# Performance work log

Hardware: AMD Instinct MI355X
Metric: run time of the kernel (lower is better)

The kernel has to match this reference:

```python
import jax, jax.numpy as jnp
import numpy as np
from jax import lax

B, T, D, LD, K = 128, 1024, 256, 512, 128
RD = LD + K  # 640 residual-LSTM width
PAD = 15     # (31 - 1) // 2 'same' padding for the LSA location conv


def _gru(x, h, wih, whh, bih, bhh):
    # torch.nn.GRUCell semantics, gate order [r, z, n]
    gi = x @ wih.T + bih
    gh = h @ whh.T + bhh
    ir, iz, inn = jnp.split(gi, 3, axis=-1)
    hr, hz, hn = jnp.split(gh, 3, axis=-1)
    r = jax.nn.sigmoid(ir + hr)
    z = jax.nn.sigmoid(iz + hz)
    n = jnp.tanh(inn + r * hn)
    return (1.0 - z) * n + z * h


def _lstm(x, h, c, wih, whh, bih, bhh):
    # torch.nn.LSTMCell semantics, gate order [i, f, g, o]
    g = x @ wih.T + bih + h @ whh.T + bhh
    i, f, gg, o = jnp.split(g, 4, axis=-1)
    c2 = jax.nn.sigmoid(f) * c + jax.nn.sigmoid(i) * jnp.tanh(gg)
    h2 = jax.nn.sigmoid(o) * jnp.tanh(c2)
    return h2, c2


def _forward(encoder_seq, encoder_seq_proj, prenet_in, attn_hidden, rnn1_h, rnn1_c,
             rnn2_h, rnn2_c, res_h, res_c, context_vec, cumulative, attn_prev,
             fc1_w, fc1_b, fc2_w, fc2_b, gru_wih, gru_whh, gru_bih, gru_bhh,
             conv_w, L_w, L_b, W_w, W_b, v_w, ri_w, ri_b,
             r1_wih, r1_whh, r1_bih, r1_bhh, r2_wih, r2_whh, r2_bih, r2_bhh,
             res_wih, res_whh, res_bih, res_bhh, stop_w, stop_b):
    # PreNet (dropout p = 0 in Decoder.__init__, so pure tanh-MLP)
    p = jnp.tanh(prenet_in @ fc1_w.T + fc1_b)
    prenet_out = jnp.tanh(p @ fc2_w.T + fc2_b)                     # [B, D//2]
    # Attention GRU
    attn_in = jnp.concatenate([context_vec, prenet_out], axis=-1)  # [B, D + D//2]
    attn_h = _gru(attn_in, attn_hidden, gru_wih, gru_whh, gru_bih, gru_bhh)  # [B, D]
    # LSA location-sensitive attention (cumulative/attn_prev are zeros at t=0)
    pq = (attn_h @ W_w.T + W_b)[:, None, :]                        # [B, 1, D]
    loc = jnp.stack([cumulative, attn_prev], axis=1)               # [B, 2, T]
    conv_out = lax.conv_general_dilated(loc, conv_w, (1,), [(PAD, PAD)],
                                        dimension_numbers=('NCH', 'OIH', 'NCH'))  # [B, 32, T]
    ploc = jnp.swapaxes(conv_out, 1, 2) @ L_w.T + L_b              # [B, T, D]
    u = jnp.squeeze(jnp.tanh(pq + encoder_seq_proj + ploc) @ v_w.T, -1)  # [B, T]
    sig = jax.nn.sigmoid(u)
    scores = sig / jnp.sum(sig, axis=1, keepdims=True)             # [B, T]
    cum_new = cumulative + scores
    context = jnp.einsum('bt,btd->bd', scores, encoder_seq)        # [B, D]
    # rnn_input projection + two residual LSTM cells (eval: no zoneout)
    x = jnp.concatenate([context, attn_h], axis=1) @ ri_w.T + ri_b  # [B, LD]
    h1, c1 = _lstm(x, rnn1_h, rnn1_c, r1_wih, r1_whh, r1_bih, r1_bhh)
    x = x + h1
    h2, c2 = _lstm(x, rnn2_h, rnn2_c, r2_wih, r2_whh, r2_bih, r2_bhh)
    x = x + h2
    # 4-layer residual LSTM stack on [prenet_in, x]
    res_x = jnp.concatenate([prenet_in, x], axis=1)                # [B, RD]
    hs, cs = [], []
    for i in range(4):
        hi, ci = _lstm(res_x, res_h[i], res_c[i], res_wih[i], res_whh[i], res_bih[i], res_bhh[i])
        res_x = res_x + hi
        hs.append(hi)
        cs.append(ci)
    cond = res_x                                                   # cond_features [B, RD]
    stop = jax.nn.sigmoid(cond @ stop_w.T + stop_b)                # [B, 1]
    return (cond, stop, scores, attn_h, h1, c1, h2, c2,
            jnp.stack(hs), jnp.stack(cs), context, cum_new)


def setup_inputs() -> dict:
    keys = iter(jax.random.split(jax.random.key(0), 64))
    nxt = lambda: next(keys)
    rn = lambda s: jax.random.normal(nxt(), s, jnp.float32)
    wp = lambda s: rn(s) * 0.02
    return {
        'encoder_seq': rn((B, T, D)),
        'encoder_seq_proj': rn((B, T, D)),
        'prenet_in': rn((B, K)),
        'attn_hidden': rn((B, D)),
        'rnn1_h': rn((B, LD)), 'rnn1_c': rn((B, LD)),
        'rnn2_h': rn((B, LD)), 'rnn2_c': rn((B, LD)),
        'res_h': rn((4, B, RD)), 'res_c': rn((4, B, RD)),
        'context_vec': rn((B, D)),
        'cumulative': jnp.zeros((B, T), jnp.float32),
        'attn_prev': jnp.zeros((B, T), jnp.float32),
        'fc1_w': wp((256, K)), 'fc1_b': jnp.zeros((256,), jnp.float32),
        'fc2_w': wp((D // 2, 256)), 'fc2_b': jnp.zeros((D // 2,), jnp.float32),
        'gru_wih': wp((3 * D, D + D // 2)), 'gru_whh': wp((3 * D, D)),
        'gru_bih': jnp.zeros((3 * D,), jnp.float32), 'gru_bhh': jnp.zeros((3 * D,), jnp.float32),
        'conv_w': wp((32, 2, 31)),
        'L_w': wp((D, 32)), 'L_b': jnp.zeros((D,), jnp.float32),
        'W_w': wp((D, D)), 'W_b': jnp.zeros((D,), jnp.float32),
        'v_w': wp((1, D)),
        'ri_w': wp((LD, 2 * D)), 'ri_b': jnp.zeros((LD,), jnp.float32),
        'r1_wih': wp((4 * LD, LD)), 'r1_whh': wp((4 * LD, LD)),
        'r1_bih': jnp.zeros((4 * LD,), jnp.float32), 'r1_bhh': jnp.zeros((4 * LD,), jnp.float32),
        'r2_wih': wp((4 * LD, LD)), 'r2_whh': wp((4 * LD, LD)),
        'r2_bih': jnp.zeros((4 * LD,), jnp.float32), 'r2_bhh': jnp.zeros((4 * LD,), jnp.float32),
        'res_wih': wp((4, 4 * RD, RD)), 'res_whh': wp((4, 4 * RD, RD)),
        'res_bih': jnp.zeros((4, 4 * RD), jnp.float32), 'res_bhh': jnp.zeros((4, 4 * RD), jnp.float32),
        'stop_w': wp((1, RD)), 'stop_b': jnp.zeros((1,), jnp.float32),
    }


def reference(encoder_seq, encoder_seq_proj, prenet_in, attn_hidden, rnn1_h, rnn1_c,
              rnn2_h, rnn2_c, res_h, res_c, context_vec, cumulative, attn_prev,
              fc1_w, fc1_b, fc2_w, fc2_b, gru_wih, gru_whh, gru_bih, gru_bhh,
              conv_w, L_w, L_b, W_w, W_b, v_w, ri_w, ri_b,
              r1_wih, r1_whh, r1_bih, r1_bhh, r2_wih, r2_whh, r2_bih, r2_bhh,
              res_wih, res_whh, res_bih, res_bhh, stop_w, stop_b):
    return _forward(encoder_seq, encoder_seq_proj, prenet_in, attn_hidden, rnn1_h, rnn1_c,
                    rnn2_h, rnn2_c, res_h, res_c, context_vec, cumulative, attn_prev,
                    fc1_w, fc1_b, fc2_w, fc2_b, gru_wih, gru_whh, gru_bih, gru_bhh,
                    conv_w, L_w, L_b, W_w, W_b, v_w, ri_w, ri_b,
                    r1_wih, r1_whh, r1_bih, r1_bhh, r2_wih, r2_whh, r2_bih, r2_bhh,
                    res_wih, res_whh, res_bih, res_bhh, stop_w, stop_b)
```

## Files before the change

kernel.cpp:

```cpp
#include <hip/hip_runtime.h>

#define DEV __device__ __forceinline__

typedef __attribute__((ext_vector_type(8))) short short8;
typedef __attribute__((ext_vector_type(4))) float f32x4;

DEV float fast_rcp(float x) { return __builtin_amdgcn_rcpf(x); }
DEV float sigm(float x) { return fast_rcp(1.0f + __expf(-x)); }
DEV float tanhf_fast(float x) { return 1.0f - 2.0f * fast_rcp(1.0f + __expf(2.0f * x)); }

DEV short f2bf(float f) {
    unsigned u = __float_as_uint(f);
    unsigned r = (u + 0x7FFFu + ((u >> 16) & 1u)) >> 16;
    return (short)r;
}

__global__ __launch_bounds__(256) void gemm2s_kernel(
    const float* __restrict__ A1, int K1, const float* __restrict__ W1, int ldw1,
    const float* __restrict__ A2, int K2, const float* __restrict__ W2, int ldw2,
    float* __restrict__ Cp, int N, int KS, int KC)
{
    __shared__ float As[2][16][128];
    __shared__ float Ws[2][16][33];
    const int tid = threadIdx.x;
    const int chunk = blockIdx.x % KS;
    const int n0 = (blockIdx.x / KS) * 32;
    const int kbeg = chunk * KC;
    const int nt = KC / 16;
    const int tx = tid & 15, ty = tid >> 4;
    const int lm = tid & 127, lk = (tid >> 7) * 8;

    float acc[16];
#pragma unroll
    for (int i = 0; i < 16; ++i) acc[i] = 0.f;

    float4 ra0, ra1, rw;
    auto load_regs = [&](int k0) {
        const float* A; const float* W; int lda, ldw, kc;
        if (k0 < K1) { A = A1; W = W1; lda = K1; ldw = ldw1; kc = k0; }
        else         { A = A2; W = W2; lda = K2; ldw = ldw2; kc = k0 - K1; }
        ra0 = *(const float4*)(A + (size_t)lm * lda + kc + lk);
        ra1 = *(const float4*)(A + (size_t)lm * lda + kc + lk + 4);
        if (tid < 128) {
            int nl = tid >> 2, kq = (tid & 3) * 4;
            rw = *(const float4*)(W + (size_t)(n0 + nl) * ldw + kc + kq);
        }
    };
    auto store_lds = [&](int buf) {
        As[buf][lk + 0][lm] = ra0.x; As[buf][lk + 1][lm] = ra0.y;
        As[buf][lk + 2][lm] = ra0.z; As[buf][lk + 3][lm] = ra0.w;
        As[buf][lk + 4][lm] = ra1.x; As[buf][lk + 5][lm] = ra1.y;
        As[buf][lk + 6][lm] = ra1.z; As[buf][lk + 7][lm] = ra1.w;
        if (tid < 128) {
            int nl = tid >> 2, kq = (tid & 3) * 4;
            Ws[buf][kq + 0][nl] = rw.x; Ws[buf][kq + 1][nl] = rw.y;
            Ws[buf][kq + 2][nl] = rw.z; Ws[buf][kq + 3][nl] = rw.w;
        }
    };

    load_regs(kbeg);
    store_lds(0);
    __syncthreads();

    for (int it = 0; it < nt; ++it) {
        const int cur = it & 1;
        if (it + 1 < nt) load_regs(kbeg + (it + 1) * 16);
#pragma unroll
        for (int kk = 0; kk < 16; ++kk) {
            float w0 = Ws[cur][kk][tx * 2 + 0];
            float w1 = Ws[cur][kk][tx * 2 + 1];
            float4 x0 = *(const float4*)&As[cur][kk][ty * 8];
            float4 x1 = *(const float4*)&As[cur][kk][ty * 8 + 4];
            acc[0] += x0.x * w0; acc[1] += x0.y * w0;
            acc[2] += x0.z * w0; acc[3] += x0.w * w0;
            acc[4] += x1.x * w0; acc[5] += x1.y * w0;
            acc[6] += x1.z * w0; acc[7] += x1.w * w0;
            acc[8]  += x0.x * w1; acc[9]  += x0.y * w1;
            acc[10] += x0.z * w1; acc[11] += x0.w * w1;
            acc[12] += x1.x * w1; acc[13] += x1.y * w1;
            acc[14] += x1.z * w1; acc[15] += x1.w * w1;
        }
        if (it + 1 < nt) store_lds(cur ^ 1);
        __syncthreads();
    }

    float* Co = Cp + (size_t)chunk * 128 * N;
#pragma unroll
    for (int j = 0; j < 2; ++j) {
        int n = n0 + tx * 2 + j;
#pragma unroll
        for (int i = 0; i < 8; ++i)
            Co[(size_t)(ty * 8 + i) * N + n] = acc[j * 8 + i];
    }
}

__global__ void reduce_act_kernel(const float* __restrict__ p, int KS, int MN,
                                  const float* __restrict__ b,
                                  float* __restrict__ out, int N, int act)
{
    int idx = blockIdx.x * 256 + threadIdx.x;
    if (idx >= MN) return;
    int n = idx % N;
    float v = b ? b[n] : 0.f;
    for (int s = 0; s < KS; ++s) v += p[(size_t)s * MN + idx];
    if (act) v = tanhf_fast(v);
    out[idx] = v;
}

__global__ void gru_gate_kernel(const float* __restrict__ gi_p, int KSi,
                                const float* __restrict__ gh_p, int KSh,
                                const float* __restrict__ bih, const float* __restrict__ bhh,
                                const float* __restrict__ h, float* __restrict__ out)
{
    const size_t MN = 128 * 768;
    int m = blockIdx.x, d = threadIdx.x;
    size_t base = (size_t)m * 768 + d;
    float ir = bih[d], iz = bih[256 + d], in = bih[512 + d];
    for (int s = 0; s < KSi; ++s) {
        const float* p = gi_p + s * MN + base;
        ir += p[0]; iz += p[256]; in += p[512];
    }
    float hr = bhh[d], hz = bhh[256 + d], hn = bhh[512 + d];
    for (int s = 0; s < KSh; ++s) {
        const float* p = gh_p + s * MN + base;
        hr += p[0]; hz += p[256]; hn += p[512];
    }
    float r = sigm(ir + hr);
    float z = sigm(iz + hz);
    float n = tanhf_fast(in + r * hn);
    out[m * 256 + d] = (1.f - z) * n + z * h[m * 256 + d];
}

__global__ void lstm_gate_kernel(const float* __restrict__ gp, int KS,
                                 const float* __restrict__ bih, const float* __restrict__ bhh,
                                 const float* __restrict__ c_in,
                                 float* __restrict__ h_out, float* __restrict__ c_out,
                                 float* __restrict__ xacc, int H)
{
    int d = blockIdx.x * 256 + threadIdx.x;
    int m = blockIdx.y;
    if (d >= H) return;
    const size_t MN = (size_t)128 * 4 * H;
    size_t base = (size_t)m * 4 * H + d;
    float iv = bih[d] + bhh[d];
    float fv = bih[H + d] + bhh[H + d];
    float gv = bih[2 * H + d] + bhh[2 * H + d];
    float ov = bih[3 * H + d] + bhh[3 * H + d];
    for (int s = 0; s < KS; ++s) {
        const float* p = gp + s * MN + base;
        iv += p[0]; fv += p[H]; gv += p[2 * H]; ov += p[3 * H];
    }
    float c2 = sigm(fv) * c_in[m * H + d] + sigm(iv) * tanhf_fast(gv);
    float h2 = sigm(ov) * tanhf_fast(c2);
    h_out[m * H + d] = h2;
    c_out[m * H + d] = c2;
    if (xacc) xacc[m * H + d] += h2;
}

__global__ void lw_bf16_kernel(const float* __restrict__ Lw, short* __restrict__ LwBf)
{
    int i = blockIdx.x * 256 + threadIdx.x;
    LwBf[i] = f2bf(Lw[i]);
}

__global__ __launch_bounds__(256) void attn_u_kernel(
    const float* __restrict__ esp, const float* __restrict__ pq,
    const short* __restrict__ LwBf, const float* __restrict__ Lb,
    const float* __restrict__ vw, const float* __restrict__ cw,
    const float* __restrict__ cum, const float* __restrict__ prev,
    float* __restrict__ sig_out)
{
    const int b = blockIdx.x >> 4;
    const int t0 = (blockIdx.x & 15) << 6;
    const int tid = threadIdx.x;

    __shared__ float cum_s[94], prev_s[94];
    __shared__ float cw_s[2][32][33];
    __shared__ short conv_bf[64 * 32];
    __shared__ short lw_bf[256 * 32];
    __shared__ float pq_s[256], vw_s[256];

    if (tid < 94) {
        int ti = t0 - 15 + tid;
        cum_s[tid] = (ti >= 0 && ti < 1024) ? cum[b * 1024 + ti] : 0.f;
    } else if (tid >= 128 && tid < 222) {
        int i = tid - 128;
        int ti = t0 - 15 + i;
        prev_s[i] = (ti >= 0 && ti < 1024) ? prev[b * 1024 + ti] : 0.f;
    }
    for (int i = tid; i < 2048; i += 256) {
        int which = i >> 10, c = (i >> 5) & 31, k = i & 31;
        cw_s[which][c][k] = (k < 31) ? cw[(c * 2 + which) * 31 + k] : 0.f;
    }
    {
        const int4* src = (const int4*)LwBf;
        int4* dst = (int4*)lw_bf;
#pragma unroll
        for (int k = 0; k < 4; ++k) dst[tid + k * 256] = src[tid + k * 256];
    }
    pq_s[tid] = pq[b * 256 + tid] + Lb[tid];
    vw_s[tid] = vw[tid];
    __syncthreads();

    {
        int c = tid & 31, t8 = (tid >> 5) << 3;
        float a[8] = {0.f, 0.f, 0.f, 0.f, 0.f, 0.f, 0.f, 0.f};
        for (int k = 0; k < 31; ++k) {
            float w0 = cw_s[0][c][k], w1 = cw_s[1][c][k];
#pragma unroll
            for (int j = 0; j < 8; ++j)
                a[j] += w0 * cum_s[t8 + j + k] + w1 * prev_s[t8 + j + k];
        }
#pragma unroll
        for (int j = 0; j < 8; ++j) conv_bf[(t8 + j) * 32 + c] = f2bf(a[j]);
    }
    __syncthreads();

    const int lane = tid & 63, w = tid >> 6;
    const int q = lane >> 4, c16 = lane & 15;
    const int myt = t0 + w * 16 + c16;

    short8 bfrag = *(const short8*)&conv_bf[(w * 16 + c16) * 32 + q * 8];
    const float* er = esp + ((size_t)(b * 1024 + myt) << 8);

    float s = 0.f;
#pragma unroll
    for (int dt = 0; dt < 16; ++dt) {
        short8 afrag = *(const short8*)&lw_bf[(dt * 16 + c16) * 32 + q * 8];
        f32x4 acc = {0.f, 0.f, 0.f, 0.f};
        acc = __builtin_amdgcn_mfma_f32_16x16x32_bf16(afrag, bfrag, acc, 0, 0, 0);
        const int d0 = dt * 16 + q * 4;
        float4 e   = *(const float4*)(er + d0);
        float4 pqv = *(const float4*)&pq_s[d0];
        float4 vwv = *(const float4*)&vw_s[d0];
        s += tanhf_fast(pqv.x + e.x + acc[0]) * vwv.x;
        s += tanhf_fast(pqv.y + e.y + acc[1]) * vwv.y;
        s += tanhf_fast(pqv.z + e.z + acc[2]) * vwv.z;
        s += tanhf_fast(pqv.w + e.w + acc[3]) * vwv.w;
    }
    s += __shfl_xor(s, 16);
    s += __shfl_xor(s, 32);
    if (lane < 16)
        sig_out[b * 1024 + t0 + w * 16 + lane] = sigm(s);
}

__global__ void attn_norm_kernel(const float* __restrict__ sig, const float* __restrict__ cum,
                                 float* __restrict__ scores, float* __restrict__ cum_new,
                                 float* __restrict__ ctx)
{
    __shared__ float red[4];
    int b = blockIdx.x, tid = threadIdx.x;
    float4 sv = *(const float4*)&sig[b * 1024 + tid * 4];
    float s = sv.x + sv.y + sv.z + sv.w;
#pragma unroll
    for (int off = 1; off < 64; off <<= 1) s += __shfl_xor(s, off);
    if ((tid & 63) == 0) red[tid >> 6] = s;
    __syncthreads();
    float inv = fast_rcp(red[0] + red[1] + red[2] + red[3]);
    float4 cv = *(const float4*)&cum[b * 1024 + tid * 4];
    float4 sc = {sv.x * inv, sv.y * inv, sv.z * inv, sv.w * inv};
    *(float4*)&scores[b * 1024 + tid * 4] = sc;
    float4 cn = {cv.x + sc.x, cv.y + sc.y, cv.z + sc.z, cv.w + sc.w};
    *(float4*)&cum_new[b * 1024 + tid * 4] = cn;
    ctx[b * 256 + tid] = 0.f;
}

__global__ void attn_ctx_kernel(const float* __restrict__ scores, const float* __restrict__ es,
                                float* __restrict__ ctx)
{
    __shared__ float sc_s[128];
    int b = blockIdx.x >> 3;
    int tbase = (blockIdx.x & 7) * 128;
    int tid = threadIdx.x;
    if (tid < 128) sc_s[tid] = scores[b * 1024 + tbase + tid];
    __syncthreads();
    float a = 0.f;
    const float* ep = es + ((size_t)(b * 1024 + tbase)) * 256 + tid;
#pragma unroll 4
    for (int tt = 0; tt < 128; ++tt)
        a += sc_s[tt] * ep[(size_t)tt * 256];
    atomicAdd(&ctx[b * 256 + tid], a);
}

__global__ void build_rescat_kernel(const float* __restrict__ pre, const float* __restrict__ x,
                                    float* __restrict__ res)
{
    int idx = blockIdx.x * 256 + threadIdx.x;
    int m = idx / 640, d = idx - m * 640;
    res[idx] = (d < 128) ? pre[m * 128 + d] : x[m * 512 + d - 128];
}

__global__ void copy_kernel(const float* __restrict__ src, float* __restrict__ dst, int n)
{
    int idx = blockIdx.x * 256 + threadIdx.x;
    if (idx < n) dst[idx] = src[idx];
}

__global__ void stop_kernel(const float* __restrict__ res, const float* __restrict__ sw,
                            const float* __restrict__ sb, float* __restrict__ stop)
{
    int m = blockIdx.x, lane = threadIdx.x;
    float s = 0.f;
    for (int k = lane; k < 640; k += 64) s += res[m * 640 + k] * sw[k];
#pragma unroll
    for (int off = 1; off < 64; off <<= 1) s += __shfl_xor(s, off);
    if (lane == 0) stop[m] = sigm(s + sb[0]);
}

extern "C" void kernel_launch(void* const* d_in, const int* in_sizes, int n_in,
                              void* d_out, int out_size, void* d_ws, size_t ws_size,
                              hipStream_t stream)
{
    const float* encoder_seq      = (const float*)d_in[0];
    const float* encoder_seq_proj = (const float*)d_in[1];
    const float* prenet_in        = (const float*)d_in[2];
    const float* attn_hidden      = (const float*)d_in[3];
    const float* rnn1_h  = (const float*)d_in[4];
    const float* rnn1_c  = (const float*)d_in[5];
    const float* rnn2_h  = (const float*)d_in[6];
    const float* rnn2_c  = (const float*)d_in[7];
    const float* res_h   = (const float*)d_in[8];
    const float* res_c   = (const float*)d_in[9];
    const float* context_vec = (const float*)d_in[10];
    const float* cumulative  = (const float*)d_in[11];
    const float* attn_prev   = (const float*)d_in[12];
    const float* fc1_w = (const float*)d_in[13];
    const float* fc1_b = (const float*)d_in[14];
    const float* fc2_w = (const float*)d_in[15];
    const float* fc2_b = (const float*)d_in[16];
    const float* gru_wih = (const float*)d_in[17];
    const float* gru_whh = (const float*)d_in[18];
    const float* gru_bih = (const float*)d_in[19];
    const float* gru_bhh = (const float*)d_in[20];
    const float* conv_w = (const float*)d_in[21];
    const float* L_w = (const float*)d_in[22];
    const float* L_b = (const float*)d_in[23];
    const float* W_w = (const float*)d_in[24];
    const float* W_b = (const float*)d_in[25];
    const float* v_w = (const float*)d_in[26];
    const float* ri_w = (const float*)d_in[27];
    const float* ri_b = (const float*)d_in[28];
    const float* r1_wih = (const float*)d_in[29];
    const float* r1_whh = (const float*)d_in[30];
    const float* r1_bih = (const float*)d_in[31];
    const float* r1_bhh = (const float*)d_in[32];
    const float* r2_wih = (const float*)d_in[33];
    const float* r2_whh = (const float*)d_in[34];
    const float* r2_bih = (const float*)d_in[35];
    const float* r2_bhh = (const float*)d_in[36];
    const float* res_wih = (const float*)d_in[37];
    const float* res_whh = (const float*)d_in[38];
    const float* res_bih = (const float*)d_in[39];
    const float* res_bhh = (const float*)d_in[40];
    const float* stop_w = (const float*)d_in[41];
    const float* stop_b = (const float*)d_in[42];

    float* ws  = (float*)d_ws;
    float* out = (float*)d_out;

    const size_t OFF_P    = 0;
    const size_t OFF_POUT = 32768;
    const size_t OFF_PQ   = 49152;
    const size_t OFF_SIG  = 81920;
    const size_t OFF_X    = 212992;
    const size_t OFF_RES  = 278528;
    const size_t OFF_LWT  = 360448;
    const size_t OFF_PART = 368640;
    const size_t OFF_PARTB = OFF_PART + (size_t)8 * 128 * 768;

    const size_t O_COND   = 0;
    const size_t O_STOP   = 81920;
    const size_t O_SCORES = 82048;
    const size_t O_ATTNH  = 213120;
    const size_t O_H1     = 245888;
    const size_t O_C1     = 311424;
    const size_t O_H2     = 376960;
    const size_t O_C2     = 442496;
    const size_t O_HS     = 508032;
    const size_t O_CS     = 835712;
    const size_t O_CTX    = 1163392;
    const size_t O_CUM    = 1196160;

    short* lwbf = (short*)(ws + OFF_LWT);
    lw_bf16_kernel<<<32, 256, 0, stream>>>(L_w, lwbf);

    gemm2s_kernel<<<8 * 4, 256, 0, stream>>>(prenet_in, 128, fc1_w, 128,
                                             nullptr, 0, nullptr, 0,
                                             ws + OFF_PART, 256, 4, 32);
    reduce_act_kernel<<<128, 256, 0, stream>>>(ws + OFF_PART, 4, 128 * 256, fc1_b,
                                               ws + OFF_P, 256, 1);
    gemm2s_kernel<<<4 * 8, 256, 0, stream>>>(ws + OFF_P, 256, fc2_w, 256,
                                             nullptr, 0, nullptr, 0,
                                             ws + OFF_PART, 128, 8, 32);
    reduce_act_kernel<<<64, 256, 0, stream>>>(ws + OFF_PART, 8, 128 * 128, fc2_b,
                                              ws + OFF_POUT, 128, 1);

    gemm2s_kernel<<<24 * 8, 256, 0, stream>>>(context_vec, 256, gru_wih, 384,
                                              ws + OFF_POUT, 128, gru_wih + 256, 384,
                                              ws + OFF_PART, 768, 8, 48);
    gemm2s_kernel<<<24 * 8, 256, 0, stream>>>(attn_hidden, 256, gru_whh, 256,
                                              nullptr, 0, nullptr, 0,
                                              ws + OFF_PARTB, 768, 8, 32);
    gru_gate_kernel<<<128, 256, 0, stream>>>(ws + OFF_PART, 8, ws + OFF_PARTB, 8,
                                             gru_bih, gru_bhh, attn_hidden, out + O_ATTNH);

    gemm2s_kernel<<<8 * 8, 256, 0, stream>>>(out + O_ATTNH, 256, W_w, 256,
                                             nullptr, 0, nullptr, 0,
                                             ws + OFF_PART, 256, 8, 32);
    reduce_act_kernel<<<128, 256, 0, stream>>>(ws + OFF_PART, 8, 128 * 256, W_b,
                                               ws + OFF_PQ, 256, 0);

    attn_u_kernel<<<2048, 256, 0, stream>>>(encoder_seq_proj, ws + OFF_PQ, lwbf,
                                            L_b, v_w, conv_w, cumulative, attn_prev,
                                            ws + OFF_SIG);
    attn_norm_kernel<<<128, 256, 0, stream>>>(ws + OFF_SIG, cumulative,
                                              out + O_SCORES, out + O_CUM, out + O_CTX);
    attn_ctx_kernel<<<1024, 256, 0, stream>>>(out + O_SCORES, encoder_seq, out + O_CTX);

    gemm2s_kernel<<<16 * 8, 256, 0, stream>>>(out + O_CTX, 256, ri_w, 512,
                                              out + O_ATTNH, 256, ri_w + 256, 512,
                                              ws + OFF_PART, 512, 8, 64);
    reduce_act_kernel<<<256, 256, 0, stream>>>(ws + OFF_PART, 8, 128 * 512, ri_b,
                                               ws + OFF_X, 512, 0);

    gemm2s_kernel<<<64 * 8, 256, 0, stream>>>(ws + OFF_X, 512, r1_wih, 512,
                                              rnn1_h, 512, r1_whh, 512,
                                              ws + OFF_PART, 2048, 8, 128);
    lstm_gate_kernel<<<dim3(2, 128), 256, 0, stream>>>(ws + OFF_PART, 8, r1_bih, r1_bhh,
                                                       rnn1_c, out + O_H1, out + O_C1,
                                                       ws + OFF_X, 512);
    gemm2s_kernel<<<64 * 8, 256, 0, stream>>>(ws + OFF_X, 512, r2_wih, 512,
                                              rnn2_h, 512, r2_whh, 512,
                                              ws + OFF_PART, 2048, 8, 128);
    lstm_gate_kernel<<<dim3(2, 128), 256, 0, stream>>>(ws + OFF_PART, 8, r2_bih, r2_bhh,
                                                       rnn2_c, out + O_H2, out + O_C2,
                                                       ws + OFF_X, 512);

    build_rescat_kernel<<<320, 256, 0, stream>>>(prenet_in, ws + OFF_X, ws + OFF_RES);

    for (int i = 0; i < 4; ++i) {
        const float* wih = res_wih + (size_t)i * 2560 * 640;
        const float* whh = res_whh + (size_t)i * 2560 * 640;
        gemm2s_kernel<<<80 * 8, 256, 0, stream>>>(ws + OFF_RES, 640, wih, 640,
                                                  res_h + (size_t)i * 81920, 640, whh, 640,
                                                  ws + OFF_PART, 2560, 8, 160);
        lstm_gate_kernel<<<dim3(3, 128), 256, 0, stream>>>(ws + OFF_PART, 8,
                                                           res_bih + (size_t)i * 2560,
                                                           res_bhh + (size_t)i * 2560,
                                                           res_c + (size_t)i * 81920,
                                                           out + O_HS + (size_t)i * 81920,
                                                           out + O_CS + (size_t)i * 81920,
                                                           ws + OFF_RES, 640);
    }

    copy_kernel<<<320, 256, 0, stream>>>(ws + OFF_RES, out + O_COND, 128 * 640);
    stop_kernel<<<128, 64, 0, stream>>>(ws + OFF_RES, stop_w, stop_b, out + O_STOP);
}
```

Before: 662.4 us.

## Replace FP32 SIMT GEMM with split-bf16 MFMA GEMM using pre-converted weights

Replaces the LDS-tiled FP32 FMA GEMM with an MFMA kernel that emulates fp32 accuracy by splitting each operand into bf16 hi and lo parts and issuing three bf16 MFMAs per tile. A new kernel converts every weight matrix to hi/lo bf16 arrays each call, and the GEMM loads fragments straight from global memory with register double-buffering instead of staging through LDS. The intent is to move the matmul work onto the matrix cores. In exchange, the weight conversion pass reads about 73 MB of fp32 and writes the same volume back as bf16 every call, which is extra memory traffic. The GRU input GEMM split is also changed to 12 K-chunks.

Result: faster. 634.2 us (-4.3%).

```diff
diff --git a/kernel.cpp b/kernel.cpp
--- a/kernel.cpp
+++ b/kernel.cpp
@@ -14,84 +14,131 @@
     unsigned r = (u + 0x7FFFu + ((u >> 16) & 1u)) >> 16;
     return (short)r;
 }
-
-__global__ __launch_bounds__(256) void gemm2s_kernel(
-    const float* __restrict__ A1, int K1, const float* __restrict__ W1, int ldw1,
-    const float* __restrict__ A2, int K2, const float* __restrict__ W2, int ldw2,
+DEV float bf2f(short h) {
+    return __uint_as_float(((unsigned)(unsigned short)h) << 16);
+}
+DEV void split1(float f, short& h, short& l) {
+    h = f2bf(f);
+    l = f2bf(f - bf2f(h));
+}
+
+__global__ __launch_bounds__(256) void convert_w_kernel(
+    const float* __restrict__ p0, const float* __restrict__ p1,
+    const float* __restrict__ p2, const float* __restrict__ p3,
+    const float* __restrict__ p4, const float* __restrict__ p5,
+    const float* __restrict__ p6, const float* __restrict__ p7,
+    const float* __restrict__ p8, const float* __restrict__ p9,
+    const float* __restrict__ p10, const float* __restrict__ p11,
+    short* __restrict__ hi, short* __restrict__ lo)
+{
+    const int c1 = 8192, c2 = 16384, c3 = 90112, c4 = 139264, c5 = 155648,
+              c6 = 221184, c7 = 483328, c8 = 745472, c9 = 1007616,
+              c10 = 1269760, c11 = 2908160, total = 4546560;
+    for (int v = blockIdx.x * 256 + threadIdx.x; v < total; v += gridDim.x * 256) {
+        const float* s = p0; int base = 0;
+        if (v >= c1)  { s = p1;  base = c1; }
+        if (v >= c2)  { s = p2;  base = c2; }
+        if (v >= c3)  { s = p3;  base = c3; }
+        if (v >= c4)  { s = p4;  base = c4; }
+        if (v >= c5)  { s = p5;  base = c5; }
+        if (v >= c6)  { s = p6;  base = c6; }
+        if (v >= c7)  { s = p7;  base = c7; }
+        if (v >= c8)  { s = p8;  base = c8; }
+        if (v >= c9)  { s = p9;  base = c9; }
+        if (v >= c10) { s = p10; base = c10; }
+        if (v >= c11) { s = p11; base = c11; }
+        float4 f = ((const float4*)s)[v - base];
+        short4 h, l;
+        split1(f.x, h.x, l.x);
+        split1(f.y, h.y, l.y);
+        split1(f.z, h.z, l.z);
+        split1(f.w, h.w, l.w);
+        ((short4*)hi)[v] = h;
+        ((short4*)lo)[v] = l;
+    }
+}
+
+__global__ __launch_bounds__(256) void gemm_mfma_kernel(
+    const float* __restrict__ A1, int K1,
+    const short* __restrict__ W1hi, const short* __restrict__ W1lo, int ldw1,
+    const float* __restrict__ A2, int K2,
+    const short* __restrict__ W2hi, const short* __restrict__ W2lo, int ldw2,
     float* __restrict__ Cp, int N, int KS, int KC)
 {
-    __shared__ float As[2][16][128];
-    __shared__ float Ws[2][16][33];
     const int tid = threadIdx.x;
     const int chunk = blockIdx.x % KS;
     const int n0 = (blockIdx.x / KS) * 32;
     const int kbeg = chunk * KC;
-    const int nt = KC / 16;
-    const int tx = tid & 15, ty = tid >> 4;
-    const int lm = tid & 127, lk = (tid >> 7) * 8;
-
-    float acc[16];
-#pragma unroll
-    for (int i = 0; i < 16; ++i) acc[i] = 0.f;
-
-    float4 ra0, ra1, rw;
-    auto load_regs = [&](int k0) {
-        const float* A; const float* W; int lda, ldw, kc;
-        if (k0 < K1) { A = A1; W = W1; lda = K1; ldw = ldw1; kc = k0; }
-        else         { A = A2; W = W2; lda = K2; ldw = ldw2; kc = k0 - K1; }
-        ra0 = *(const float4*)(A + (size_t)lm * lda + kc + lk);
-        ra1 = *(const float4*)(A + (size_t)lm * lda + kc + lk + 4);
-        if (tid < 128) {
-            int nl = tid >> 2, kq = (tid & 3) * 4;
-            rw = *(const float4*)(W + (size_t)(n0 + nl) * ldw + kc + kq);
+    const int w = tid >> 6, lane = tid & 63;
+    const int q = lane >> 4, r = lane & 15;
+    const int m_base = w * 32;
+
+    f32x4 acc[2][2];
+#pragma unroll
+    for (int mt = 0; mt < 2; ++mt)
+#pragma unroll
+        for (int nt = 0; nt < 2; ++nt)
+            acc[mt][nt] = (f32x4){0.f, 0.f, 0.f, 0.f};
+
+    auto load_frag = [&](int kg, float4 (&a)[2][2], short8 (&bh)[2], short8 (&bl)[2]) {
+        const float* A; const short *Wh, *Wl; int lda, ldw, kc;
+        if (kg < K1) { A = A1; Wh = W1hi; Wl = W1lo; lda = K1; ldw = ldw1; kc = kg; }
+        else         { A = A2; Wh = W2hi; Wl = W2lo; lda = K2; ldw = ldw2; kc = kg - K1; }
+#pragma unroll
+        for (int mt = 0; mt < 2; ++mt) {
+            const float* ap = A + (size_t)(m_base + mt * 16 + r) * lda + kc + q * 8;
+            a[mt][0] = *(const float4*)ap;
+            a[mt][1] = *(const float4*)(ap + 4);
+        }
+#pragma unroll
+        for (int nt = 0; nt < 2; ++nt) {
+            size_t off = (size_t)(n0 + nt * 16 + r) * ldw + kc + q * 8;
+            bh[nt] = *(const short8*)(Wh + off);
+            bl[nt] = *(const short8*)(Wl + off);
         }
     };
-    auto store_lds = [&](int buf) {
-        As[buf][lk + 0][lm] = ra0.x; As[buf][lk + 1][lm] = ra0.y;
-        As[buf][lk + 2][lm] = ra0.z; As[buf][lk + 3][lm] = ra0.w;
-        As[buf][lk + 4][lm] = ra1.x; As[buf][lk + 5][lm] = ra1.y;
-        As[buf][lk + 6][lm] = ra1.z; As[buf][lk + 7][lm] = ra1.w;
-        if (tid < 128) {
-            int nl = tid >> 2, kq = (tid & 3) * 4;
-            Ws[buf][kq + 0][nl] = rw.x; Ws[buf][kq + 1][nl] = rw.y;
-            Ws[buf][kq + 2][nl] = rw.z; Ws[buf][kq + 3][nl] = rw.w;
+
+    auto compute = [&](const float4 (&a)[2][2], const short8 (&bh)[2], const short8 (&bl)[2]) {
+#pragma unroll
+        for (int mt = 0; mt < 2; ++mt) {
+            float fv[8] = {a[mt][0].x, a[mt][0].y, a[mt][0].z, a[mt][0].w,
+                           a[mt][1].x, a[mt][1].y, a[mt][1].z, a[mt][1].w};
+            short8 ah, al;
+#pragma unroll
+            for (int j = 0; j < 8; ++j) {
+                short h, l;
+                split1(fv[j], h, l);
+                ah[j] = h; al[j] = l;
+            }
+#pragma unroll
+            for (int nt = 0; nt < 2; ++nt) {
+                acc[mt][nt] = __builtin_amdgcn_mfma_f32_16x16x32_bf16(ah, bh[nt], acc[mt][nt], 0, 0, 0);
+                acc[mt][nt] = __builtin_amdgcn_mfma_f32_16x16x32_bf16(al, bh[nt], acc[mt][nt], 0, 0, 0);
+                acc[mt][nt] = __builtin_amdgcn_mfma_f32_16x16x32_bf16(ah, bl[nt], acc[mt][nt], 0, 0, 0);
+            }
         }
     };
 
-    load_regs(kbeg);
-    store_lds(0);
-    __syncthreads();
-
-    for (int it = 0; it < nt; ++it) {
-        const int cur = it & 1;
-        if (it + 1 < nt) load_regs(kbeg + (it + 1) * 16);
-#pragma unroll
-        for (int kk = 0; kk < 16; ++kk) {
-            float w0 = Ws[cur][kk][tx * 2 + 0];
-            float w1 = Ws[cur][kk][tx * 2 + 1];
-            float4 x0 = *(const float4*)&As[cur][kk][ty * 8];
-            float4 x1 = *(const float4*)&As[cur][kk][ty * 8 + 4];
-            acc[0] += x0.x * w0; acc[1] += x0.y * w0;
-            acc[2] += x0.z * w0; acc[3] += x0.w * w0;
-            acc[4] += x1.x * w0; acc[5] += x1.y * w0;
-            acc[6] += x1.z * w0; acc[7] += x1.w * w0;
-            acc[8]  += x0.x * w1; acc[9]  += x0.y * w1;
-            acc[10] += x0.z * w1; acc[11] += x0.w * w1;
-            acc[12] += x1.x * w1; acc[13] += x1.y * w1;
-            acc[14] += x1.z * w1; acc[15] += x1.w * w1;
-        }
-        if (it + 1 < nt) store_lds(cur ^ 1);
-        __syncthreads();
-    }
+    float4 a0[2][2], a1[2][2];
+    short8 bh0[2], bl0[2], bh1[2], bl1[2];
+    const int nsteps = KC >> 5;
+
+    load_frag(kbeg, a0, bh0, bl0);
+    for (int s = 0; s + 1 < nsteps; ++s) {
+        if (s & 1) { load_frag(kbeg + (s + 1) * 32, a0, bh0, bl0); compute(a1, bh1, bl1); }
+        else       { load_frag(kbeg + (s + 1) * 32, a1, bh1, bl1); compute(a0, bh0, bl0); }
+    }
+    if ((nsteps - 1) & 1) compute(a1, bh1, bl1);
+    else                  compute(a0, bh0, bl0);
 
     float* Co = Cp + (size_t)chunk * 128 * N;
 #pragma unroll
-    for (int j = 0; j < 2; ++j) {
-        int n = n0 + tx * 2 + j;
-#pragma unroll
-        for (int i = 0; i < 8; ++i)
-            Co[(size_t)(ty * 8 + i) * N + n] = acc[j * 8 + i];
-    }
+    for (int mt = 0; mt < 2; ++mt)
+#pragma unroll
+        for (int nt = 0; nt < 2; ++nt)
+#pragma unroll
+            for (int i = 0; i < 4; ++i)
+                Co[(size_t)(m_base + mt * 16 + q * 4 + i) * N + n0 + nt * 16 + r] = acc[mt][nt][i];
 }
 
 __global__ void reduce_act_kernel(const float* __restrict__ p, int KS, int MN,
@@ -366,7 +413,16 @@
     const size_t OFF_RES  = 278528;
     const size_t OFF_LWT  = 360448;
     const size_t OFF_PART = 368640;
-    const size_t OFF_PARTB = OFF_PART + (size_t)8 * 128 * 768;
+    const size_t OFF_PARTB = OFF_PART + (size_t)12 * 128 * 768;
+    const size_t OFF_WBF  = 4000000;
+
+    const size_t WOFF_FC1 = 0,        WOFF_FC2 = 32768,   WOFF_GI = 65536,
+                 WOFF_GH  = 360448,   WOFF_WW  = 557056,  WOFF_RI = 622592,
+                 WOFF_R1I = 884736,   WOFF_R1H = 1933312, WOFF_R2I = 2981888,
+                 WOFF_R2H = 4030464,  WOFF_RESI = 5079040, WOFF_RESH = 11632640,
+                 W_TOTAL  = 18186240;
+    short* WHI = (short*)(ws + OFF_WBF);
+    short* WLO = WHI + W_TOTAL;
 
     const size_t O_COND   = 0;
     const size_t O_STOP   = 81920;
@@ -381,32 +437,41 @@
     const size_t O_CTX    = 1163392;
     const size_t O_CUM    = 1196160;
 
+    convert_w_kernel<<<2048, 256, 0, stream>>>(
+        fc1_w, fc2_w, gru_wih, gru_whh, W_w, ri_w,
+        r1_wih, r1_whh, r2_wih, r2_whh, res_wih, res_whh, WHI, WLO);
+
     short* lwbf = (short*)(ws + OFF_LWT);
     lw_bf16_kernel<<<32, 256, 0, stream>>>(L_w, lwbf);
 
-    gemm2s_kernel<<<8 * 4, 256, 0, stream>>>(prenet_in, 128, fc1_w, 128,
-                                             nullptr, 0, nullptr, 0,
-                                             ws + OFF_PART, 256, 4, 32);
+    gemm_mfma_kernel<<<8 * 4, 256, 0, stream>>>(
+        prenet_in, 128, WHI + WOFF_FC1, WLO + WOFF_FC1, 128,
+        nullptr, 0, nullptr, nullptr, 0,
+        ws + OFF_PART, 256, 4, 32);
     reduce_act_kernel<<<128, 256, 0, stream>>>(ws + OFF_PART, 4, 128 * 256, fc1_b,
                                                ws + OFF_P, 256, 1);
-    gemm2s_kernel<<<4 * 8, 256, 0, stream>>>(ws + OFF_P, 256, fc2_w, 256,
-                                             nullptr, 0, nullptr, 0,
-                                             ws + OFF_PART, 128, 8, 32);
+    gemm_mfma_kernel<<<4 * 8, 256, 0, stream>>>(
+        ws + OFF_P, 256, WHI + WOFF_FC2, WLO + WOFF_FC2, 256,
+        nullptr, 0, nullptr, nullptr, 0,
+        ws + OFF_PART, 128, 8, 32);
     reduce_act_kernel<<<64, 256, 0, stream>>>(ws + OFF_PART, 8, 128 * 128, fc2_b,
                                               ws + OFF_POUT, 128, 1);
 
-    gemm2s_kernel<<<24 * 8, 256, 0, stream>>>(context_vec, 256, gru_wih, 384,
-                                              ws + OFF_POUT, 128, gru_wih + 256, 384,
-                                              ws + OFF_PART, 768, 8, 48);
-    gemm2s_kernel<<<24 * 8, 256, 0, stream>>>(attn_hidden, 256, gru_whh, 256,
-                                              nullptr, 0, nullptr, 0,
-                                              ws + OFF_PARTB, 768, 8, 32);
-    gru_gate_kernel<<<128, 256, 0, stream>>>(ws + OFF_PART, 8, ws + OFF_PARTB, 8,
+    gemm_mfma_kernel<<<24 * 12, 256, 0, stream>>>(
+        context_vec, 256, WHI + WOFF_GI, WLO + WOFF_GI, 384,
+        ws + OFF_POUT, 128, WHI + WOFF_GI + 256, WLO + WOFF_GI + 256, 384,
+        ws + OFF_PART, 768, 12, 32);
+    gemm_mfma_kernel<<<24 * 8, 256, 0, stream>>>(
+        attn_hidden, 256, WHI + WOFF_GH, WLO + WOFF_GH, 256,
+        nullptr, 0, nullptr, nullptr, 0,
+        ws + OFF_PARTB, 768, 8, 32);
+    gru_gate_kernel<<<128, 256, 0, stream>>>(ws + OFF_PART, 12, ws + OFF_PARTB, 8,
                                              gru_bih, gru_bhh, attn_hidden, out + O_ATTNH);
 
-    gemm2s_kernel<<<8 * 8, 256, 0, stream>>>(out + O_ATTNH, 256, W_w, 256,
-                                             nullptr, 0, nullptr, 0,
-                                             ws + OFF_PART, 256, 8, 32);
+    gemm_mfma_kernel<<<8 * 8, 256, 0, stream>>>(
+        out + O_ATTNH, 256, WHI + WOFF_WW, WLO + WOFF_WW, 256,
+        nullptr, 0, nullptr, nullptr, 0,
+        ws + OFF_PART, 256, 8, 32);
     reduce_act_kernel<<<128, 256, 0, stream>>>(ws + OFF_PART, 8, 128 * 256, W_b,
                                                ws + OFF_PQ, 256, 0);
 
@@ -417,21 +482,24 @@
                                               out + O_SCORES, out + O_CUM, out + O_CTX);
     attn_ctx_kernel<<<1024, 256, 0, stream>>>(out + O_SCORES, encoder_seq, out + O_CTX);
 
-    gemm2s_kernel<<<16 * 8, 256, 0, stream>>>(out + O_CTX, 256, ri_w, 512,
-                                              out + O_ATTNH, 256, ri_w + 256, 512,
-                                              ws + OFF_PART, 512, 8, 64);
+    gemm_mfma_kernel<<<16 * 8, 256, 0, stream>>>(
+        out + O_CTX, 256, WHI + WOFF_RI, WLO + WOFF_RI, 512,
+        out + O_ATTNH, 256, WHI + WOFF_RI + 256, WLO + WOFF_RI + 256, 512,
+        ws + OFF_PART, 512, 8, 64);
     reduce_act_kernel<<<256, 256, 0, stream>>>(ws + OFF_PART, 8, 128 * 512, ri_b,
                                                ws + OFF_X, 512, 0);
 
-    gemm2s_kernel<<<64 * 8, 256, 0, stream>>>(ws + OFF_X, 512, r1_wih, 512,
-                                              rnn1_h, 512, r1_whh, 512,
-                                              ws + OFF_PART, 2048, 8, 128);
+    gemm_mfma_kernel<<<64 * 8, 256, 0, stream>>>(
+        ws + OFF_X, 512, WHI + WOFF_R1I, WLO + WOFF_R1I, 512,
+        rnn1_h, 512, WHI + WOFF_R1H, WLO + WOFF_R1H, 512,
+        ws + OFF_PART, 2048, 8, 128);
     lstm_gate_kernel<<<dim3(2, 128), 256, 0, stream>>>(ws + OFF_PART, 8, r1_bih, r1_bhh,
                                                        rnn1_c, out + O_H1, out + O_C1,
                                                        ws + OFF_X, 512);
-    gemm2s_kernel<<<64 * 8, 256, 0, stream>>>(ws + OFF_X, 512, r2_wih, 512,
-                                              rnn2_h, 512, r2_whh, 512,
-                                              ws + OFF_PART, 2048, 8, 128);
+    gemm_mfma_kernel<<<64 * 8, 256, 0, stream>>>(
+        ws + OFF_X, 512, WHI + WOFF_R2I, WLO + WOFF_R2I, 512,
+        rnn2_h, 512, WHI + WOFF_R2H, WLO + WOFF_R2H, 512,
+        ws + OFF_PART, 2048, 8, 128);
     lstm_gate_kernel<<<dim3(2, 128), 256, 0, stream>>>(ws + OFF_PART, 8, r2_bih, r2_bhh,
                                                        rnn2_c, out + O_H2, out + O_C2,
                                                        ws + OFF_X, 512);
@@ -439,11 +507,14 @@
     build_rescat_kernel<<<320, 256, 0, stream>>>(prenet_in, ws + OFF_X, ws + OFF_RES);
 
     for (int i = 0; i < 4; ++i) {
-        const float* wih = res_wih + (size_t)i * 2560 * 640;
-        const float* whh = res_whh + (size_t)i * 2560 * 640;
-        gemm2s_kernel<<<80 * 8, 256, 0, stream>>>(ws + OFF_RES, 640, wih, 640,
-                                                  res_h + (size_t)i * 81920, 640, whh, 640,
-                                                  ws + OFF_PART, 2560, 8, 160);
+        const short* wih_hi = WHI + WOFF_RESI + (size_t)i * 2560 * 640;
+        const short* wih_lo = WLO + WOFF_RESI + (size_t)i * 2560 * 640;
+        const short* whh_hi = WHI + WOFF_RESH + (size_t)i * 2560 * 640;
+        const short* whh_lo = WLO + WOFF_RESH + (size_t)i * 2560 * 640;
+        gemm_mfma_kernel<<<80 * 8, 256, 0, stream>>>(
+            ws + OFF_RES, 640, wih_hi, wih_lo, 640,
+            res_h + (size_t)i * 81920, 640, whh_hi, whh_lo, 640,
+            ws + OFF_PART, 2560, 8, 160);
         lstm_gate_kernel<<<dim3(3, 128), 256, 0, stream>>>(ws + OFF_PART, 8,
                                                            res_bih + (size_t)i * 2560,
                                                            res_bhh + (size_t)i * 2560,
```
